# Optimization experiments

Hardware: AMD Instinct MI355X
Metric: run time of the kernel (lower is better)

## Reference

```python
import jax, jax.numpy as jnp
import numpy as np

N_NODES = 50000
N_EDGES = 500000
NFEAT = 128
NHID = 128
NOUT = 16


def setup_inputs() -> dict:
    key = jax.random.key(0)
    ks = jax.random.split(key, 8)
    x = jax.random.normal(ks[0], (N_NODES, NFEAT), dtype=jnp.float32)
    edge_src = jax.random.randint(ks[1], (N_EDGES,), 0, N_NODES, dtype=jnp.int32)
    edge_dst = jax.random.randint(ks[2], (N_EDGES,), 0, N_NODES, dtype=jnp.int32)
    edge_weight = jax.random.uniform(ks[3], (N_EDGES,), dtype=jnp.float32)
    # Glorot-ish init for linear weights, zero bias (PyG GCNConv default bias=0)
    def glorot(k, fan_in, fan_out):
        s = jnp.sqrt(6.0 / (fan_in + fan_out))
        return jax.random.uniform(k, (fan_in, fan_out), jnp.float32, -s, s)
    W1 = glorot(ks[4], NFEAT, NHID)
    W2 = glorot(ks[5], NHID, NHID)
    W3 = glorot(ks[6], NHID, NOUT)
    b1 = jnp.zeros((NHID,), jnp.float32)
    b2 = jnp.zeros((NHID,), jnp.float32)
    b3 = jnp.zeros((NOUT,), jnp.float32)
    return {"x": x, "edge_src": edge_src, "edge_dst": edge_dst,
            "edge_weight": edge_weight, "W1": W1, "b1": b1,
            "W2": W2, "b2": b2, "W3": W3, "b3": b3}


def gcn_conv(x, src, dst, ew, W, b):
    """PyG GCNConv: symmetric-normalized aggregation with self-loops (weight 1).

    out_i = sum_{(j->i)} d_i^{-1/2} w_ji d_j^{-1/2} (x_j W) + d_i^{-1} (x_i W) + b
    where d_i = 1 + sum of incoming edge weights.
    """
    n = x.shape[0]
    xw = x @ W                                            # [N, F_out]
    deg = jax.ops.segment_sum(ew, dst, num_segments=n) + 1.0  # self-loop weight 1
    dinv = jnp.where(deg > 0, jax.lax.rsqrt(deg), 0.0)    # d^{-1/2}
    norm = dinv[src] * ew * dinv[dst]                     # [E]
    agg = jax.ops.segment_sum(xw[src] * norm[:, None], dst, num_segments=n)
    self_loop = xw * (dinv * dinv)[:, None]               # d_i^{-1} * x_i W
    return agg + self_loop + b


def reference(x, edge_src, edge_dst, edge_weight, W1, b1, W2, b2, W3, b3):
    # Dropout layers are identity in eval mode.
    h = gcn_conv(x, edge_src, edge_dst, edge_weight, W1, b1)
    h = jax.nn.relu(h)
    h = gcn_conv(h, edge_src, edge_dst, edge_weight, W2, b2)
    h = jax.nn.relu(h)
    h = gcn_conv(h, edge_src, edge_dst, edge_weight, W3, b3)
    return jax.nn.log_softmax(h, axis=1)
```

## Files before the change

### kernel.cpp

```cpp
#include <hip/hip_runtime.h>
#include <math.h>

#define NN 50000
#define NE 500000
#define NF 128
#define NO 16
#define SCAN_B 1024
#define NPART 16
#define EBL 1954

typedef _Float16 f16x8 __attribute__((ext_vector_type(8)));
typedef float f32x4 __attribute__((ext_vector_type(4)));


__global__ void k_count_rank(const int* __restrict__ dst, int* __restrict__ pcnt,
                             int* __restrict__ rank, int E,
                             const float* __restrict__ W1, const float* __restrict__ W2,
                             _Float16* __restrict__ W1T, _Float16* __restrict__ W2T) {
    int b = blockIdx.x;
    if (b < EBL) {
        int part = b & (NPART - 1);
        int e = b * 256 + threadIdx.x;
        if (e < E) {
            int d = dst[e];
            rank[e] = atomicAdd(&pcnt[part * NN + d], 1);
        }
    } else {
        int idx = (b - EBL) * 256 + threadIdx.x;
        int r = idx >> 7, c = idx & 127;
        W1T[(size_t)c * NF + r] = (_Float16)W1[idx];
        W2T[(size_t)c * NF + r] = (_Float16)W2[idx];
    }
}

__global__ void k_scan1f(int* __restrict__ pcnt, int* __restrict__ offs_p,
                         int* __restrict__ bsums, int N) {
    __shared__ int sm[SCAN_B];
    int t = threadIdx.x;
    int i = blockIdx.x * SCAN_B + t;
    int c = 0;
    if (i < N) {
        int run = 0;
#pragma unroll
        for (int p = 0; p < NPART; ++p) {
            int v = pcnt[p * NN + i];
            pcnt[p * NN + i] = run;
            run += v;
        }
        c = run;
    }
    sm[t] = c;
    __syncthreads();
    for (int off = 1; off < SCAN_B; off <<= 1) {
        int x = (t >= off) ? sm[t - off] : 0;
        __syncthreads();
        sm[t] += x;
        __syncthreads();
    }
    if (i < N) offs_p[i] = sm[t] - c;
    if (t == SCAN_B - 1) bsums[blockIdx.x] = sm[t];
}

__global__ void k_scan2(int* __restrict__ bsums, int NB) {
    int t = threadIdx.x;
    int v = (t < NB) ? bsums[t] : 0;
    int orig = v;
#pragma unroll
    for (int off = 1; off < 64; off <<= 1) {
        int u = __shfl_up(v, off, 64);
        if (t >= off) v += u;
    }
    if (t < NB) bsums[t] = v - orig;
}

__global__ void k_scan3x(const int* __restrict__ offs_p, const int* __restrict__ bsums,
                         int* __restrict__ pcnt, int* __restrict__ offs_f, int E) {
    int i = blockIdx.x * blockDim.x + threadIdx.x;
    if (i < NPART * NN) {
        int p = i / NN;
        int n = i - p * NN;
        int v = offs_p[n] + bsums[n >> 10];
        pcnt[i] += v;
        if (p == 0) offs_f[n] = v;
    } else if (i == NPART * NN) {
        offs_f[NN] = E;
    }
}

__global__ void k_scatter(const int* __restrict__ src, const int* __restrict__ dst,
                          const float* __restrict__ ew, const int* __restrict__ pcnt,
                          const int* __restrict__ rank, int2* __restrict__ edge_rec, int E) {
    int part = blockIdx.x & (NPART - 1);
    int e = blockIdx.x * blockDim.x + threadIdx.x;
    if (e < E) {
        int d = dst[e];
        int pos = pcnt[part * NN + d] + rank[e];
        int2 r;
        r.x = src[e];
        r.y = __float_as_int(ew[e]);
        edge_rec[pos] = r;
    }
}

__global__ void k_dinv_csr(const int2* __restrict__ edge_rec, const int* __restrict__ offs,
                           float* __restrict__ dinv, int N) {
    int n = blockIdx.x * blockDim.x + threadIdx.x;
    if (n < N) {
        float deg = 1.0f;
        int s = offs[n], e = offs[n + 1];
        for (int j = s; j < e; ++j) deg += __int_as_float(edge_rec[j].y);
        dinv[n] = rsqrtf(deg);
    }
}


__device__ inline f16x8 afrag_load(const float* X, int row, int k0) {
    const float4* p = (const float4*)(X + (size_t)row * NF + k0);
    float4 a = p[0], b = p[1];
    f16x8 r;
    r[0] = (_Float16)a.x; r[1] = (_Float16)a.y; r[2] = (_Float16)a.z; r[3] = (_Float16)a.w;
    r[4] = (_Float16)b.x; r[5] = (_Float16)b.y; r[6] = (_Float16)b.z; r[7] = (_Float16)b.w;
    return r;
}
__device__ inline f16x8 afrag_load(const _Float16* X, int row, int k0) {
    return *(const f16x8*)(X + (size_t)row * NF + k0);
}

template <typename TA>
__global__ __launch_bounds__(256) void k_gemm_mfma(const TA* __restrict__ X,
                                                   const _Float16* __restrict__ WT,
                                                   const float* __restrict__ dinv,
                                                   _Float16* __restrict__ Z, int M) {
    __shared__ _Float16 ls[4][16 * NF];
    const int tid  = threadIdx.x;
    const int w    = tid >> 6;
    const int lane = tid & 63;
    const int n16  = lane & 15;
    const int quad = lane >> 4;
    const int r0   = blockIdx.x * 64 + w * 16;

    int arow = r0 + n16; if (arow > M - 1) arow = M - 1;

    f32x4 acc[8];
#pragma unroll
    for (int c = 0; c < 8; ++c) acc[c] = (f32x4){0.f, 0.f, 0.f, 0.f};

#pragma unroll
    for (int kk = 0; kk < 4; ++kk) {
        int k0 = kk * 32 + quad * 8;
        f16x8 a = afrag_load(X, arow, k0);
#pragma unroll
        for (int c = 0; c < 8; ++c) {
            f16x8 b = *(const f16x8*)(WT + (size_t)(c * 16 + n16) * NF + k0);
            acc[c] = __builtin_amdgcn_mfma_f32_16x16x32_f16(a, b, acc[c], 0, 0, 0);
        }
    }

#pragma unroll
    for (int reg = 0; reg < 4; ++reg) {
        int lrow = quad * 4 + reg;
        int grow = r0 + lrow; if (grow > M - 1) grow = M - 1;
        float di = dinv[grow];
#pragma unroll
        for (int c = 0; c < 8; ++c)
            ls[w][lrow * NF + c * 16 + n16] = (_Float16)(acc[c][reg] * di);
    }
    __syncthreads();
#pragma unroll
    for (int i = 0; i < 4; ++i) {
        int off16 = i * 64 + lane;
        int row = off16 >> 4;
        int grow = r0 + row;
        if (grow < M) {
            f16x8 v = *(const f16x8*)(&ls[w][off16 * 8]);
            *(f16x8*)(Z + (size_t)grow * NF + (off16 & 15) * 8) = v;
        }
    }
}

__global__ __launch_bounds__(256) void k_agg128h(const _Float16* __restrict__ z,
                                                 const float* __restrict__ dinv,
                                                 const int* __restrict__ offs,
                                                 const int2* __restrict__ edge_rec,
                                                 const float* __restrict__ bias,
                                                 _Float16* __restrict__ hout, int relu) {
    const int tid = threadIdx.x;
    const int ln = tid & 63;
    int n = __builtin_amdgcn_readfirstlane(blockIdx.x * 4 + (tid >> 6));

    union CV { unsigned int u; _Float16 h[2]; };

    float di = dinv[n];
    CV sv; sv.u = *(const unsigned int*)(z + ((size_t)n << 7) + ln * 2);
    float acc0 = (float)sv.h[0];
    float acc1 = (float)sv.h[1];

    int s = offs[n], e = offs[n + 1];
    for (int base = s; base < e; base += 64) {
        int cnt = e - base; if (cnt > 64) cnt = 64;
        int2 rec = {0, 0};
        if (ln < cnt) rec = edge_rec[base + ln];
        int   my_s = rec.x;
        float my_w = __int_as_float(rec.y);
        int k = 0;
        for (; k + 3 < cnt; k += 4) {
            int s0 = __shfl(my_s, k, 64),     s1 = __shfl(my_s, k + 1, 64);
            int s2 = __shfl(my_s, k + 2, 64), s3 = __shfl(my_s, k + 3, 64);
            float w0 = __shfl(my_w, k, 64),     w1 = __shfl(my_w, k + 1, 64);
            float w2 = __shfl(my_w, k + 2, 64), w3 = __shfl(my_w, k + 3, 64);
            CV u0, u1, u2, u3;
            u0.u = *(const unsigned int*)(z + ((size_t)s0 << 7) + ln * 2);
            u1.u = *(const unsigned int*)(z + ((size_t)s1 << 7) + ln * 2);
            u2.u = *(const unsigned int*)(z + ((size_t)s2 << 7) + ln * 2);
            u3.u = *(const unsigned int*)(z + ((size_t)s3 << 7) + ln * 2);
            acc0 = fmaf((float)u0.h[0], w0, acc0); acc1 = fmaf((float)u0.h[1], w0, acc1);
            acc0 = fmaf((float)u1.h[0], w1, acc0); acc1 = fmaf((float)u1.h[1], w1, acc1);
            acc0 = fmaf((float)u2.h[0], w2, acc0); acc1 = fmaf((float)u2.h[1], w2, acc1);
            acc0 = fmaf((float)u3.h[0], w3, acc0); acc1 = fmaf((float)u3.h[1], w3, acc1);
        }
        for (; k < cnt; ++k) {
            int   s0 = __shfl(my_s, k, 64);
            float w0 = __shfl(my_w, k, 64);
            CV u0; u0.u = *(const unsigned int*)(z + ((size_t)s0 << 7) + ln * 2);
            acc0 = fmaf((float)u0.h[0], w0, acc0);
            acc1 = fmaf((float)u0.h[1], w0, acc1);
        }
    }
    float2 bb = *(const float2*)(bias + ln * 2);
    acc0 = fmaf(di, acc0, bb.x);
    acc1 = fmaf(di, acc1, bb.y);
    if (relu) { acc0 = fmaxf(acc0, 0.0f); acc1 = fmaxf(acc1, 0.0f); }
    CV o; o.h[0] = (_Float16)acc0; o.h[1] = (_Float16)acc1;
    *(unsigned int*)(hout + ((size_t)n << 7) + ln * 2) = o.u;
}

__global__ __launch_bounds__(256) void k_gemm16(const _Float16* __restrict__ H,
                                                const float* __restrict__ W3,
                                                const float* __restrict__ dinv,
                                                _Float16* __restrict__ Z3, int M) {
    __shared__ float Wl[NF * NO];
    __shared__ float Hs[16 * 132];
    int tid = threadIdx.x;
    for (int i = tid; i < NF * NO; i += 256) Wl[i] = W3[i];
    int n0 = blockIdx.x * 16;
    {
        int row = tid >> 4, h8 = tid & 15;
        int gr = n0 + row; if (gr > M - 1) gr = M - 1;
        f16x8 v = *(const f16x8*)(H + (size_t)gr * NF + h8 * 8);
        float4 f0 = {(float)v[0], (float)v[1], (float)v[2], (float)v[3]};
        float4 f1 = {(float)v[4], (float)v[5], (float)v[6], (float)v[7]};
        *(float4*)(&Hs[row * 132 + h8 * 8])     = f0;
        *(float4*)(&Hs[row * 132 + h8 * 8 + 4]) = f1;
    }
    __syncthreads();
    int ln = tid >> 4, c = tid & 15;
    float acc = 0.0f;
#pragma unroll 8
    for (int k = 0; k < NF; ++k) acc = fmaf(Hs[ln * 132 + k], Wl[k * NO + c], acc);
    int n = n0 + ln;
    if (n < M) Z3[(size_t)n * NO + c] = (_Float16)(acc * dinv[n]);
}

__global__ __launch_bounds__(256) void k_agg16_ls(const _Float16* __restrict__ z3,
                                                  const float* __restrict__ dinv,
                                                  const int* __restrict__ offs,
                                                  const int2* __restrict__ edge_rec,
                                                  const float* __restrict__ bias,
                                                  float* __restrict__ out) {
    int tid = threadIdx.x;
    int ln = tid >> 4, c = tid & 15;
    int n = blockIdx.x * 16 + ln;
    float acc = (float)z3[(size_t)n * NO + c];
    int s = offs[n], e = offs[n + 1];
    int j = s;
    for (; j + 1 < e; j += 2) {
        int2 r0 = edge_rec[j], r1 = edge_rec[j + 1];
        acc = fmaf((float)z3[((size_t)r0.x << 4) + c], __int_as_float(r0.y), acc);
        acc = fmaf((float)z3[((size_t)r1.x << 4) + c], __int_as_float(r1.y), acc);
    }
    if (j < e) {
        int2 r0 = edge_rec[j];
        acc = fmaf((float)z3[((size_t)r0.x << 4) + c], __int_as_float(r0.y), acc);
    }
    acc = fmaf(dinv[n], acc, bias[c]);
    float m = acc;
#pragma unroll
    for (int off = 8; off > 0; off >>= 1) m = fmaxf(m, __shfl_xor(m, off, 16));
    float ex = expf(acc - m);
    float ss = ex;
#pragma unroll
    for (int off = 8; off > 0; off >>= 1) ss += __shfl_xor(ss, off, 16);
    out[(size_t)n * NO + c] = acc - m - logf(ss);
}


extern "C" void kernel_launch(void* const* d_in, const int* in_sizes, int n_in,
                              void* d_out, int out_size, void* d_ws, size_t ws_size,
                              hipStream_t stream) {
    const float* x   = (const float*)d_in[0];
    const int*   esrc= (const int*)  d_in[1];
    const int*   edst= (const int*)  d_in[2];
    const float* ew  = (const float*)d_in[3];
    const float* W1  = (const float*)d_in[4];
    const float* b1  = (const float*)d_in[5];
    const float* W2  = (const float*)d_in[6];
    const float* b2  = (const float*)d_in[7];
    const float* W3  = (const float*)d_in[8];
    const float* b3  = (const float*)d_in[9];
    float* out = (float*)d_out;

    char* p = (char*)d_ws;
    _Float16* z   = (_Float16*)p; p += (size_t)NN * NF * 2;
    _Float16* h   = (_Float16*)p; p += (size_t)NN * NF * 2;
    _Float16* z3  = (_Float16*)p; p += (size_t)NN * NO * 2;
    float* dinv   = (float*)p; p += (size_t)NN * 4;
    int2*  edge_rec = (int2*)p; p += (size_t)NE * 8;
    int*   rank   = (int*)p;   p += (size_t)NE * 4;
    int*   pcnt   = (int*)p;   p += (size_t)NPART * NN * 4;
    int*   offs_p = (int*)p;   p += (size_t)(NN + 1) * 4;
    int*   offs_f = (int*)p;   p += (size_t)(NN + 1) * 4;
    int*   bsums  = (int*)p;   p += 256;
    _Float16* W1T = (_Float16*)p; p += (size_t)NF * NF * 2;
    _Float16* W2T = (_Float16*)p; p += (size_t)NF * NF * 2;

    const int NB  = (NN + SCAN_B - 1) / SCAN_B;
    const int NBL = (NN + 255) / 256;

    hipMemsetAsync(pcnt, 0, (size_t)NPART * NN * 4, stream);

    k_count_rank<<<EBL + 64, 256, 0, stream>>>(edst, pcnt, rank, NE, W1, W2, W1T, W2T);
    k_scan1f<<<NB, SCAN_B, 0, stream>>>(pcnt, offs_p, bsums, NN);
    k_scan2<<<1, 64, 0, stream>>>(bsums, NB);
    k_scan3x<<<(NPART * NN + 256) / 256, 256, 0, stream>>>(offs_p, bsums, pcnt, offs_f, NE);
    k_scatter<<<EBL, 256, 0, stream>>>(esrc, edst, ew, pcnt, rank, edge_rec, NE);
    k_dinv_csr<<<NBL, 256, 0, stream>>>(edge_rec, offs_f, dinv, NN);

    k_gemm_mfma<float><<<(NN + 63) / 64, 256, 0, stream>>>(x, W1T, dinv, z, NN);
    k_agg128h<<<NN / 4, 256, 0, stream>>>(z, dinv, offs_f, edge_rec, b1, h, 1);
    k_gemm_mfma<_Float16><<<(NN + 63) / 64, 256, 0, stream>>>(h, W2T, dinv, z, NN);
    k_agg128h<<<NN / 4, 256, 0, stream>>>(z, dinv, offs_f, edge_rec, b2, h, 1);
    k_gemm16<<<(NN + 15) / 16, 256, 0, stream>>>(h, W3, dinv, z3, NN);
    k_agg16_ls<<<NN / 16, 256, 0, stream>>>(z3, dinv, offs_f, edge_rec, b3, out);
}
```

Baseline: 252.3 us.

## Slice feature matrices into 16-column panels and pack edge records to 32 bits

```diff
diff --git a/kernel.cpp b/kernel.cpp
--- a/kernel.cpp
+++ b/kernel.cpp
@@ -5,12 +5,22 @@
 #define NE 500000
 #define NF 128
 #define NO 16
+#define NSL 8
 #define SCAN_B 1024
 #define NPART 16
 #define EBL 1954
 
+static_assert(NN < 65536, "src must fit u16");
+
 typedef _Float16 f16x8 __attribute__((ext_vector_type(8)));
 typedef float f32x4 __attribute__((ext_vector_type(4)));
+
+union HU { unsigned short u; _Float16 h; };
+
+__device__ inline float rec_w(unsigned int rec) {
+    HU cu; cu.u = (unsigned short)(rec >> 16);
+    return (float)cu.h;
+}
 
 
 __global__ void k_count_rank(const int* __restrict__ dst, int* __restrict__ pcnt,
@@ -89,32 +99,30 @@
 
 __global__ void k_scatter(const int* __restrict__ src, const int* __restrict__ dst,
                           const float* __restrict__ ew, const int* __restrict__ pcnt,
-                          const int* __restrict__ rank, int2* __restrict__ edge_rec, int E) {
+                          const int* __restrict__ rank, unsigned int* __restrict__ erec, int E) {
     int part = blockIdx.x & (NPART - 1);
     int e = blockIdx.x * blockDim.x + threadIdx.x;
     if (e < E) {
         int d = dst[e];
         int pos = pcnt[part * NN + d] + rank[e];
-        int2 r;
-        r.x = src[e];
-        r.y = __float_as_int(ew[e]);
-        edge_rec[pos] = r;
-    }
-}
-
-__global__ void k_dinv_csr(const int2* __restrict__ edge_rec, const int* __restrict__ offs,
+        HU cu; cu.h = (_Float16)ew[e];
+        erec[pos] = (unsigned int)src[e] | ((unsigned int)cu.u << 16);
+    }
+}
+
+__global__ void k_dinv_csr(const unsigned int* __restrict__ erec, const int* __restrict__ offs,
                            float* __restrict__ dinv, int N) {
     int n = blockIdx.x * blockDim.x + threadIdx.x;
     if (n < N) {
         float deg = 1.0f;
         int s = offs[n], e = offs[n + 1];
-        for (int j = s; j < e; ++j) deg += __int_as_float(edge_rec[j].y);
+        for (int j = s; j < e; ++j) deg += rec_w(erec[j]);
         dinv[n] = rsqrtf(deg);
     }
 }
 
 
-__device__ inline f16x8 afrag_load(const float* X, int row, int k0) {
+__device__ inline f16x8 afrag_load_f32(const float* X, int row, int k0) {
     const float4* p = (const float4*)(X + (size_t)row * NF + k0);
     float4 a = p[0], b = p[1];
     f16x8 r;
@@ -122,16 +130,13 @@
     r[4] = (_Float16)b.x; r[5] = (_Float16)b.y; r[6] = (_Float16)b.z; r[7] = (_Float16)b.w;
     return r;
 }
-__device__ inline f16x8 afrag_load(const _Float16* X, int row, int k0) {
-    return *(const f16x8*)(X + (size_t)row * NF + k0);
-}
-
-template <typename TA>
+
+template <typename TA, bool ASLICE>
 __global__ __launch_bounds__(256) void k_gemm_mfma(const TA* __restrict__ X,
                                                    const _Float16* __restrict__ WT,
                                                    const float* __restrict__ dinv,
                                                    _Float16* __restrict__ Z, int M) {
-    __shared__ _Float16 ls[4][16 * NF];
+    __shared__ _Float16 ls[4][16 * 136];
     const int tid  = threadIdx.x;
     const int w    = tid >> 6;
     const int lane = tid & 63;
@@ -148,7 +153,13 @@
 #pragma unroll
     for (int kk = 0; kk < 4; ++kk) {
         int k0 = kk * 32 + quad * 8;
-        f16x8 a = afrag_load(X, arow, k0);
+        f16x8 a;
+        if constexpr (ASLICE) {
+            int s = k0 >> 4;
+            a = *(const f16x8*)(X + (((size_t)s * NN + arow) << 4) + (k0 & 15));
+        } else {
+            a = afrag_load_f32(X, arow, k0);
+        }
 #pragma unroll
         for (int c = 0; c < 8; ++c) {
             f16x8 b = *(const f16x8*)(WT + (size_t)(c * 16 + n16) * NF + k0);
@@ -163,75 +174,55 @@
         float di = dinv[grow];
 #pragma unroll
         for (int c = 0; c < 8; ++c)
-            ls[w][lrow * NF + c * 16 + n16] = (_Float16)(acc[c][reg] * di);
+            ls[w][lrow * 136 + c * 16 + n16] = (_Float16)(acc[c][reg] * di);
     }
     __syncthreads();
 #pragma unroll
-    for (int i = 0; i < 4; ++i) {
-        int off16 = i * 64 + lane;
-        int row = off16 >> 4;
+    for (int it = 0; it < 4; ++it) {
+        int s   = it * 2 + (lane >> 5);
+        int row = (lane >> 1) & 15;
+        int fc  = lane & 1;
         int grow = r0 + row;
         if (grow < M) {
-            f16x8 v = *(const f16x8*)(&ls[w][off16 * 8]);
-            *(f16x8*)(Z + (size_t)grow * NF + (off16 & 15) * 8) = v;
-        }
-    }
-}
-
-__global__ __launch_bounds__(256) void k_agg128h(const _Float16* __restrict__ z,
-                                                 const float* __restrict__ dinv,
-                                                 const int* __restrict__ offs,
-                                                 const int2* __restrict__ edge_rec,
-                                                 const float* __restrict__ bias,
-                                                 _Float16* __restrict__ hout, int relu) {
-    const int tid = threadIdx.x;
-    const int ln = tid & 63;
-    int n = __builtin_amdgcn_readfirstlane(blockIdx.x * 4 + (tid >> 6));
-
-    union CV { unsigned int u; _Float16 h[2]; };
-
-    float di = dinv[n];
-    CV sv; sv.u = *(const unsigned int*)(z + ((size_t)n << 7) + ln * 2);
-    float acc0 = (float)sv.h[0];
-    float acc1 = (float)sv.h[1];
-
-    int s = offs[n], e = offs[n + 1];
-    for (int base = s; base < e; base += 64) {
-        int cnt = e - base; if (cnt > 64) cnt = 64;
-        int2 rec = {0, 0};
-        if (ln < cnt) rec = edge_rec[base + ln];
-        int   my_s = rec.x;
-        float my_w = __int_as_float(rec.y);
-        int k = 0;
-        for (; k + 3 < cnt; k += 4) {
-            int s0 = __shfl(my_s, k, 64),     s1 = __shfl(my_s, k + 1, 64);
-            int s2 = __shfl(my_s, k + 2, 64), s3 = __shfl(my_s, k + 3, 64);
-            float w0 = __shfl(my_w, k, 64),     w1 = __shfl(my_w, k + 1, 64);
-            float w2 = __shfl(my_w, k + 2, 64), w3 = __shfl(my_w, k + 3, 64);
-            CV u0, u1, u2, u3;
-            u0.u = *(const unsigned int*)(z + ((size_t)s0 << 7) + ln * 2);
-            u1.u = *(const unsigned int*)(z + ((size_t)s1 << 7) + ln * 2);
-            u2.u = *(const unsigned int*)(z + ((size_t)s2 << 7) + ln * 2);
-            u3.u = *(const unsigned int*)(z + ((size_t)s3 << 7) + ln * 2);
-            acc0 = fmaf((float)u0.h[0], w0, acc0); acc1 = fmaf((float)u0.h[1], w0, acc1);
-            acc0 = fmaf((float)u1.h[0], w1, acc0); acc1 = fmaf((float)u1.h[1], w1, acc1);
-            acc0 = fmaf((float)u2.h[0], w2, acc0); acc1 = fmaf((float)u2.h[1], w2, acc1);
-            acc0 = fmaf((float)u3.h[0], w3, acc0); acc1 = fmaf((float)u3.h[1], w3, acc1);
-        }
-        for (; k < cnt; ++k) {
-            int   s0 = __shfl(my_s, k, 64);
-            float w0 = __shfl(my_w, k, 64);
-            CV u0; u0.u = *(const unsigned int*)(z + ((size_t)s0 << 7) + ln * 2);
-            acc0 = fmaf((float)u0.h[0], w0, acc0);
-            acc1 = fmaf((float)u0.h[1], w0, acc1);
-        }
-    }
-    float2 bb = *(const float2*)(bias + ln * 2);
-    acc0 = fmaf(di, acc0, bb.x);
-    acc1 = fmaf(di, acc1, bb.y);
-    if (relu) { acc0 = fmaxf(acc0, 0.0f); acc1 = fmaxf(acc1, 0.0f); }
-    CV o; o.h[0] = (_Float16)acc0; o.h[1] = (_Float16)acc1;
-    *(unsigned int*)(hout + ((size_t)n << 7) + ln * 2) = o.u;
+            f16x8 v = *(const f16x8*)(&ls[w][row * 136 + s * 16 + fc * 8]);
+            *(f16x8*)(Z + (((size_t)s * NN + grow) << 4) + fc * 8) = v;
+        }
+    }
+}
+
+__global__ __launch_bounds__(256) void k_agg_slice(const _Float16* __restrict__ z_s,
+                                                   const float* __restrict__ dinv,
+                                                   const int* __restrict__ offs,
+                                                   const unsigned int* __restrict__ erec,
+                                                   const float* __restrict__ bias,
+                                                   _Float16* __restrict__ h_s, int relu) {
+    const int tid   = threadIdx.x;
+    const int lane  = tid & 63;
+    const int f     = lane & 15;
+    const int eslot = lane >> 4;
+    const int slice = blockIdx.x & (NSL - 1);
+    const int n     = (blockIdx.x >> 3) * 4 + (tid >> 6);
+
+    const size_t sbase = ((size_t)slice * NN) << 4;
+
+    int s0 = offs[n], e0 = offs[n + 1];
+    float acc = 0.0f;
+    for (int j0 = s0; j0 < e0; j0 += 4) {
+        int idx = j0 + eslot;
+        unsigned int rec = 0u;
+        if (idx < e0) rec = erec[idx];
+        int sn = rec & 0xFFFF;
+        float wv = rec_w(rec);
+        float val = (float)z_s[sbase + ((size_t)sn << 4) + f];
+        acc = fmaf(val, wv, acc);
+    }
+    acc += __shfl_xor(acc, 16, 64);
+    acc += __shfl_xor(acc, 32, 64);
+
+    float self = (float)z_s[sbase + ((size_t)n << 4) + f];
+    float r = fmaf(dinv[n], self + acc, bias[slice * 16 + f]);
+    if (relu) r = fmaxf(r, 0.0f);
+    if (eslot == 0) h_s[sbase + ((size_t)n << 4) + f] = (_Float16)r;
 }
 
 __global__ __launch_bounds__(256) void k_gemm16(const _Float16* __restrict__ H,
@@ -246,7 +237,8 @@
     {
         int row = tid >> 4, h8 = tid & 15;
         int gr = n0 + row; if (gr > M - 1) gr = M - 1;
-        f16x8 v = *(const f16x8*)(H + (size_t)gr * NF + h8 * 8);
+        int s = h8 >> 1, off = (h8 & 1) * 8;
+        f16x8 v = *(const f16x8*)(H + (((size_t)s * NN + gr) << 4) + off);
         float4 f0 = {(float)v[0], (float)v[1], (float)v[2], (float)v[3]};
         float4 f1 = {(float)v[4], (float)v[5], (float)v[6], (float)v[7]};
         *(float4*)(&Hs[row * 132 + h8 * 8])     = f0;
@@ -264,23 +256,23 @@
 __global__ __launch_bounds__(256) void k_agg16_ls(const _Float16* __restrict__ z3,
                                                   const float* __restrict__ dinv,
                                                   const int* __restrict__ offs,
-                                                  const int2* __restrict__ edge_rec,
+                                                  const unsigned int* __restrict__ erec,
                                                   const float* __restrict__ bias,
                                                   float* __restrict__ out) {
     int tid = threadIdx.x;
     int ln = tid >> 4, c = tid & 15;
     int n = blockIdx.x * 16 + ln;
-    float acc = (float)z3[(size_t)n * NO + c];
+    float acc = (float)z3[((size_t)n << 4) + c];
     int s = offs[n], e = offs[n + 1];
     int j = s;
     for (; j + 1 < e; j += 2) {
-        int2 r0 = edge_rec[j], r1 = edge_rec[j + 1];
-        acc = fmaf((float)z3[((size_t)r0.x << 4) + c], __int_as_float(r0.y), acc);
-        acc = fmaf((float)z3[((size_t)r1.x << 4) + c], __int_as_float(r1.y), acc);
+        unsigned int r0 = erec[j], r1 = erec[j + 1];
+        acc = fmaf((float)z3[((size_t)(r0 & 0xFFFF) << 4) + c], rec_w(r0), acc);
+        acc = fmaf((float)z3[((size_t)(r1 & 0xFFFF) << 4) + c], rec_w(r1), acc);
     }
     if (j < e) {
-        int2 r0 = edge_rec[j];
-        acc = fmaf((float)z3[((size_t)r0.x << 4) + c], __int_as_float(r0.y), acc);
+        unsigned int r0 = erec[j];
+        acc = fmaf((float)z3[((size_t)(r0 & 0xFFFF) << 4) + c], rec_w(r0), acc);
     }
     acc = fmaf(dinv[n], acc, bias[c]);
     float m = acc;
@@ -314,7 +306,7 @@
     _Float16* h   = (_Float16*)p; p += (size_t)NN * NF * 2;
     _Float16* z3  = (_Float16*)p; p += (size_t)NN * NO * 2;
     float* dinv   = (float*)p; p += (size_t)NN * 4;
-    int2*  edge_rec = (int2*)p; p += (size_t)NE * 8;
+    unsigned int* erec = (unsigned int*)p; p += (size_t)NE * 4;
     int*   rank   = (int*)p;   p += (size_t)NE * 4;
     int*   pcnt   = (int*)p;   p += (size_t)NPART * NN * 4;
     int*   offs_p = (int*)p;   p += (size_t)(NN + 1) * 4;
@@ -332,13 +324,14 @@
     k_scan1f<<<NB, SCAN_B, 0, stream>>>(pcnt, offs_p, bsums, NN);
     k_scan2<<<1, 64, 0, stream>>>(bsums, NB);
     k_scan3x<<<(NPART * NN + 256) / 256, 256, 0, stream>>>(offs_p, bsums, pcnt, offs_f, NE);
-    k_scatter<<<EBL, 256, 0, stream>>>(esrc, edst, ew, pcnt, rank, edge_rec, NE);
-    k_dinv_csr<<<NBL, 256, 0, stream>>>(edge_rec, offs_f, dinv, NN);
-
-    k_gemm_mfma<float><<<(NN + 63) / 64, 256, 0, stream>>>(x, W1T, dinv, z, NN);
-    k_agg128h<<<NN / 4, 256, 0, stream>>>(z, dinv, offs_f, edge_rec, b1, h, 1);
-    k_gemm_mfma<_Float16><<<(NN + 63) / 64, 256, 0, stream>>>(h, W2T, dinv, z, NN);
-    k_agg128h<<<NN / 4, 256, 0, stream>>>(z, dinv, offs_f, edge_rec, b2, h, 1);
+    k_scatter<<<EBL, 256, 0, stream>>>(esrc, edst, ew, pcnt, rank, erec, NE);
+    k_dinv_csr<<<NBL, 256, 0, stream>>>(erec, offs_f, dinv, NN);
+
+    const int AGG_GRID = (NN / 4) * NSL;
+    k_gemm_mfma<float, false><<<(NN + 63) / 64, 256, 0, stream>>>(x, W1T, dinv, z, NN);
+    k_agg_slice<<<AGG_GRID, 256, 0, stream>>>(z, dinv, offs_f, erec, b1, h, 1);
+    k_gemm_mfma<_Float16, true><<<(NN + 63) / 64, 256, 0, stream>>>(h, W2T, dinv, z, NN);
+    k_agg_slice<<<AGG_GRID, 256, 0, stream>>>(z, dinv, offs_f, erec, b2, h, 1);
     k_gemm16<<<(NN + 15) / 16, 256, 0, stream>>>(h, W3, dinv, z3, NN);
-    k_agg16_ls<<<NN / 16, 256, 0, stream>>>(z3, dinv, offs_f, edge_rec, b3, out);
-}
+    k_agg16_ls<<<NN / 16, 256, 0, stream>>>(z3, dinv, offs_f, erec, b3, out);
+}
```

After: 426.0 us. 1.69x slower.
